# Performance work log

Measured on AMD Instinct MI355X. Metric: run time of the kernel, lower is better.

## Reference

```python
import jax, jax.numpy as jnp
import numpy as np

PATCH = 15  # box-filter kernel size (odd -> SAME padding == padding=PATCH//2, stride 1)


def _box_filter(x, k):
    """All-ones kxk conv2d, stride 1, zero pad k//2. x: (N,1,H,W).
    The ones kernel is separable: ones(k,k) = ones(k,1) @ ones(1,k)."""
    dn = ('NCHW', 'OIHW', 'NCHW')
    kh = jnp.ones((1, 1, k, 1), x.dtype)
    kw = jnp.ones((1, 1, 1, k), x.dtype)
    x = jax.lax.conv_general_dilated(x, kh, (1, 1), 'SAME', dimension_numbers=dn)
    x = jax.lax.conv_general_dilated(x, kw, (1, 1), 'SAME', dimension_numbers=dn)
    return x


def _rgb_to_yuv420(rgb):
    """rgb: (N,3,H,W) -> y:(N,H,W), u,v:(N,H/2,W/2) (2x2 avg-pooled chroma)."""
    r, g, b = rgb[:, 0], rgb[:, 1], rgb[:, 2]
    y = 0.299 * r + 0.587 * g + 0.114 * b
    u = -0.169 * r - 0.331 * g + 0.5 * b + 128.0
    v = 0.5 * r - 0.46 * g - 0.04 * b + 128.0
    n, h, w = u.shape
    u = u.reshape(n, h // 2, 2, w // 2, 2).mean(axis=(2, 4))
    v = v.reshape(n, h // 2, 2, w // 2, 2).mean(axis=(2, 4))
    return y, u, v


def _filtered_channels(img, k):
    y, u, v = _rgb_to_yuv420(img)
    return (_box_filter(y[:, None], k),
            _box_filter(u[:, None], k),
            _box_filter(v[:, None], k))


def setup_inputs() -> dict:
    key = jax.random.key(0)
    k1, k2 = jax.random.split(key)
    input_ = jax.random.uniform(k1, (16, 3, 512, 512), dtype=jnp.float32)
    target = jax.random.uniform(k2, (16, 3, 512, 512), dtype=jnp.float32)
    return {"input": input_, "target": target}


def reference(input, target):
    yi, ui, vi = _filtered_channels(input, PATCH)
    yt, ut, vt = _filtered_channels(target, PATCH)
    mse = lambda a, b: jnp.mean((a - b) ** 2)
    return mse(yi, yt) + mse(ui, ut) + mse(vi, vt)
```

## Files before the change

kernel.cpp:

```cpp
#include <hip/hip_runtime.h>

#define NIMG 16
#define H 512
#define W 512
#define CH 256
#define CW 256
#define HALF 7

__global__ void diff_hbox_kernel(const float* __restrict__ in, const float* __restrict__ tgt,
                                 float* __restrict__ hY, float* __restrict__ hUV) {
    __shared__ float sY0[W + 16], sY1[W + 16], sU[CW + 16], sV[CW + 16];
    const int tid = threadIdx.x;
    const int cy = blockIdx.x & (CH - 1);
    const int n  = blockIdx.x >> 8;

    if (tid < 8) {
        sY0[tid] = 0.f; sY0[W + 8 + tid] = 0.f;
        sY1[tid] = 0.f; sY1[W + 8 + tid] = 0.f;
        sU[tid] = 0.f;  sU[CW + 8 + tid] = 0.f;
        sV[tid] = 0.f;  sV[CW + 8 + tid] = 0.f;
    }

    const size_t plane = (size_t)H * W;
    const float* pi = in  + (size_t)n * 3 * plane;
    const float* pt = tgt + (size_t)n * 3 * plane;

    const int y0 = cy << 1;
    const int x0 = tid << 1;
    const size_t o0 = (size_t)y0 * W + x0;
    const size_t o1 = o0 + W;

    float2 ir0 = *(const float2*)(pi + o0);
    float2 ir1 = *(const float2*)(pi + o1);
    float2 ig0 = *(const float2*)(pi + plane + o0);
    float2 ig1 = *(const float2*)(pi + plane + o1);
    float2 ib0 = *(const float2*)(pi + 2 * plane + o0);
    float2 ib1 = *(const float2*)(pi + 2 * plane + o1);

    float2 tr0 = *(const float2*)(pt + o0);
    float2 tr1 = *(const float2*)(pt + o1);
    float2 tg0 = *(const float2*)(pt + plane + o0);
    float2 tg1 = *(const float2*)(pt + plane + o1);
    float2 tb0 = *(const float2*)(pt + 2 * plane + o0);
    float2 tb1 = *(const float2*)(pt + 2 * plane + o1);

    float dr00 = ir0.x - tr0.x, dr01 = ir0.y - tr0.y;
    float dr10 = ir1.x - tr1.x, dr11 = ir1.y - tr1.y;
    float dg00 = ig0.x - tg0.x, dg01 = ig0.y - tg0.y;
    float dg10 = ig1.x - tg1.x, dg11 = ig1.y - tg1.y;
    float db00 = ib0.x - tb0.x, db01 = ib0.y - tb0.y;
    float db10 = ib1.x - tb1.x, db11 = ib1.y - tb1.y;

    sY0[8 + x0]     = 0.299f * dr00 + 0.587f * dg00 + 0.114f * db00;
    sY0[8 + x0 + 1] = 0.299f * dr01 + 0.587f * dg01 + 0.114f * db01;
    sY1[8 + x0]     = 0.299f * dr10 + 0.587f * dg10 + 0.114f * db10;
    sY1[8 + x0 + 1] = 0.299f * dr11 + 0.587f * dg11 + 0.114f * db11;

    float sr = dr00 + dr01 + dr10 + dr11;
    float sg = dg00 + dg01 + dg10 + dg11;
    float sb = db00 + db01 + db10 + db11;
    sU[8 + tid] = (-0.169f * sr - 0.331f * sg + 0.5f * sb) * 0.25f;
    sV[8 + tid] = ( 0.5f   * sr - 0.46f  * sg - 0.04f * sb) * 0.25f;

    __syncthreads();

    {
        const int row = tid >> 7;
        const int xb  = (tid & 127) << 2;
        const float* srow = row ? sY1 : sY0;
        float s = 0.f;
#pragma unroll
        for (int j = 1; j <= 15; ++j) s += srow[xb + j];
        float4 o;
        o.x = s; s += srow[xb + 16] - srow[xb + 1];
        o.y = s; s += srow[xb + 17] - srow[xb + 2];
        o.z = s; s += srow[xb + 18] - srow[xb + 3];
        o.w = s;
        *(float4*)(hY + ((size_t)n * H + y0 + row) * W + xb) = o;
    }

    {
        const int uv = tid >> 7;
        const int t  = tid & 127;
        const int xb = t << 1;
        const float* srow = uv ? sV : sU;
        float s = 0.f;
#pragma unroll
        for (int j = 1; j <= 15; ++j) s += srow[xb + j];
        float2 o;
        o.x = s; s += srow[xb + 16] - srow[xb + 1];
        o.y = s;
        const size_t p = (size_t)(n * 2 + uv);
        *(float2*)(hUV + (p * CH + cy) * CW + xb) = o;
    }
}

__global__ void vbox_sq_partial_kernel(const float* __restrict__ hY,
                                       const float* __restrict__ hUV,
                                       int gY, float invY, float invC,
                                       float* __restrict__ partials) {
    const int b = blockIdx.x;
    const float* src; int wShift, hMask; float inv; int idx;
    if (b < gY) {
        src = hY; wShift = 9; hMask = H - 1; inv = invY;
        idx = b * 256 + threadIdx.x;
    } else {
        src = hUV; wShift = 8; hMask = CH - 1; inv = invC;
        idx = (b - gY) * 256 + threadIdx.x;
    }
    const int y = (idx >> wShift) & hMask;
    const float* col = src + (idx - (y << wShift));
    float s = 0.f;
#pragma unroll
    for (int t = -HALF; t <= HALF; ++t) {
        int yy = y + t;
        int yc = min(max(yy, 0), hMask);
        float v = col[(size_t)yc << wShift];
        s += (yy == yc) ? v : 0.f;
    }
    float val = s * s;

    for (int o = 32; o > 0; o >>= 1) val += __shfl_down(val, o, 64);
    __shared__ float partial[4];
    const int lane = threadIdx.x & 63, wid = threadIdx.x >> 6;
    if (lane == 0) partial[wid] = val;
    __syncthreads();
    if (threadIdx.x == 0) {
        float t = partial[0] + partial[1] + partial[2] + partial[3];
        partials[b] = t * inv;
    }
}

__global__ void final_reduce_kernel(const float* __restrict__ partials, int n,
                                    float* __restrict__ out) {
    float s = 0.f;
    for (int i = threadIdx.x; i < n; i += 1024) s += partials[i];
    for (int o = 32; o > 0; o >>= 1) s += __shfl_down(s, o, 64);
    __shared__ float partial[16];
    const int lane = threadIdx.x & 63, wid = threadIdx.x >> 6;
    if (lane == 0) partial[wid] = s;
    __syncthreads();
    if (threadIdx.x == 0) {
        float t = 0.f;
#pragma unroll
        for (int i = 0; i < 16; ++i) t += partial[i];
        *out = t;
    }
}

extern "C" void kernel_launch(void* const* d_in, const int* in_sizes, int n_in,
                              void* d_out, int out_size, void* d_ws, size_t ws_size,
                              hipStream_t stream) {
    const float* input  = (const float*)d_in[0];
    const float* target = (const float*)d_in[1];
    float* out = (float*)d_out;

    const size_t yElems = (size_t)NIMG * H * W;
    const size_t cElems = (size_t)NIMG * CH * CW;

    float* ws = (float*)d_ws;
    float* hY       = ws;
    float* hUV      = hY + yElems;
    float* partials = hUV + 2 * cElems;

    const int gY  = (int)(yElems / 256);
    const int gUV = (int)(2 * cElems / 256);
    const int nPart = gY + gUV;

    diff_hbox_kernel<<<NIMG * CH, 256, 0, stream>>>(input, target, hY, hUV);

    vbox_sq_partial_kernel<<<gY + gUV, 256, 0, stream>>>(
        hY, hUV, gY, 1.0f / (float)yElems, 1.0f / (float)cElems, partials);

    final_reduce_kernel<<<1, 1024, 0, stream>>>(partials, nPart, out);
}
```

Measured before the change: 150.0 us.

## Store intermediates as bf16 and fuse vertical box with last-block reduction

The horizontally filtered intermediates are now stored as bf16, which halves the workspace traffic between the two passes. The vertical box pass becomes a running-sum sweep over 128-row chunks per column in only 192 blocks, instead of 15 reads per output element. The separate final reduce kernel is replaced by an atomic counter and last-block reduction, plus a memset of the counter. This trades precision in the intermediates and leaves the vertical pass with low parallelism and a serial dependency down each column.

```diff
diff --git a/kernel.cpp b/kernel.cpp
--- a/kernel.cpp
+++ b/kernel.cpp
@@ -7,8 +7,18 @@
 #define CW 256
 #define HALF 7
 
+static __device__ __forceinline__ unsigned short f2bf(float f) {
+    unsigned u = __float_as_uint(f);
+    u += 0x7FFFu + ((u >> 16) & 1u);
+    return (unsigned short)(u >> 16);
+}
+static __device__ __forceinline__ float bf2f(unsigned short h) {
+    return __uint_as_float(((unsigned)h) << 16);
+}
+
 __global__ void diff_hbox_kernel(const float* __restrict__ in, const float* __restrict__ tgt,
-                                 float* __restrict__ hY, float* __restrict__ hUV) {
+                                 unsigned short* __restrict__ hY,
+                                 unsigned short* __restrict__ hUV) {
     __shared__ float sY0[W + 16], sY1[W + 16], sU[CW + 16], sV[CW + 16];
     const int tid = threadIdx.x;
     const int cy = blockIdx.x & (CH - 1);
@@ -71,12 +81,12 @@
         float s = 0.f;
 #pragma unroll
         for (int j = 1; j <= 15; ++j) s += srow[xb + j];
-        float4 o;
-        o.x = s; s += srow[xb + 16] - srow[xb + 1];
-        o.y = s; s += srow[xb + 17] - srow[xb + 2];
-        o.z = s; s += srow[xb + 18] - srow[xb + 3];
-        o.w = s;
-        *(float4*)(hY + ((size_t)n * H + y0 + row) * W + xb) = o;
+        ushort4 o;
+        o.x = f2bf(s); s += srow[xb + 16] - srow[xb + 1];
+        o.y = f2bf(s); s += srow[xb + 17] - srow[xb + 2];
+        o.z = f2bf(s); s += srow[xb + 18] - srow[xb + 3];
+        o.w = f2bf(s);
+        *(ushort4*)(hY + ((size_t)n * H + y0 + row) * W + xb) = o;
     }
 
     {
@@ -87,64 +97,90 @@
         float s = 0.f;
 #pragma unroll
         for (int j = 1; j <= 15; ++j) s += srow[xb + j];
-        float2 o;
-        o.x = s; s += srow[xb + 16] - srow[xb + 1];
-        o.y = s;
+        ushort2 o;
+        o.x = f2bf(s); s += srow[xb + 16] - srow[xb + 1];
+        o.y = f2bf(s);
         const size_t p = (size_t)(n * 2 + uv);
-        *(float2*)(hUV + (p * CH + cy) * CW + xb) = o;
-    }
-}
-
-__global__ void vbox_sq_partial_kernel(const float* __restrict__ hY,
-                                       const float* __restrict__ hUV,
-                                       int gY, float invY, float invC,
-                                       float* __restrict__ partials) {
+        *(ushort2*)(hUV + (p * CH + cy) * CW + xb) = o;
+    }
+}
+
+#define NBLK 192
+__global__ void vbox_finish_kernel(const unsigned short* __restrict__ hY,
+                                   const unsigned short* __restrict__ hUV,
+                                   float invY, float invC,
+                                   float* __restrict__ partials,
+                                   unsigned* __restrict__ counter,
+                                   float* __restrict__ out) {
     const int b = blockIdx.x;
-    const float* src; int wShift, hMask; float inv; int idx;
-    if (b < gY) {
-        src = hY; wShift = 9; hMask = H - 1; inv = invY;
-        idx = b * 256 + threadIdx.x;
+    float acc = 0.f;
+    if (b < 128) {
+        const int img   = b >> 3;
+        const int strip = (b >> 2) & 1;
+        const int chunk = b & 3;
+        const int x = (strip << 8) + threadIdx.x;
+        const unsigned short* col = hY + ((size_t)img << 18) + x;
+        const int y0 = chunk << 7;
+        float s = 0.f;
+#pragma unroll
+        for (int t = -HALF; t <= HALF; ++t) {
+            int yy = y0 + t;
+            s += ((unsigned)yy < (unsigned)H) ? bf2f(col[yy << 9]) : 0.f;
+        }
+        for (int i = 0; i < 128; ++i) {
+            const int y = y0 + i;
+            acc += s * s;
+            const int ya = y + HALF + 1, yr = y - HALF;
+            float va = ((unsigned)ya < (unsigned)H) ? bf2f(col[ya << 9]) : 0.f;
+            float vr = ((unsigned)yr < (unsigned)H) ? bf2f(col[yr << 9]) : 0.f;
+            s += va - vr;
+        }
+        acc *= invY;
     } else {
-        src = hUV; wShift = 8; hMask = CH - 1; inv = invC;
-        idx = (b - gY) * 256 + threadIdx.x;
-    }
-    const int y = (idx >> wShift) & hMask;
-    const float* col = src + (idx - (y << wShift));
-    float s = 0.f;
-#pragma unroll
-    for (int t = -HALF; t <= HALF; ++t) {
-        int yy = y + t;
-        int yc = min(max(yy, 0), hMask);
-        float v = col[(size_t)yc << wShift];
-        s += (yy == yc) ? v : 0.f;
-    }
-    float val = s * s;
-
-    for (int o = 32; o > 0; o >>= 1) val += __shfl_down(val, o, 64);
-    __shared__ float partial[4];
+        const int bb = b - 128;
+        const int plane = bb >> 1;
+        const int chunk = bb & 1;
+        const int x = threadIdx.x;
+        const unsigned short* col = hUV + ((size_t)plane << 16) + x;
+        const int y0 = chunk << 7;
+        float s = 0.f;
+#pragma unroll
+        for (int t = -HALF; t <= HALF; ++t) {
+            int yy = y0 + t;
+            s += ((unsigned)yy < (unsigned)CH) ? bf2f(col[yy << 8]) : 0.f;
+        }
+        for (int i = 0; i < 128; ++i) {
+            const int y = y0 + i;
+            acc += s * s;
+            const int ya = y + HALF + 1, yr = y - HALF;
+            float va = ((unsigned)ya < (unsigned)CH) ? bf2f(col[ya << 8]) : 0.f;
+            float vr = ((unsigned)yr < (unsigned)CH) ? bf2f(col[yr << 8]) : 0.f;
+            s += va - vr;
+        }
+        acc *= invC;
+    }
+
+    for (int o = 32; o > 0; o >>= 1) acc += __shfl_down(acc, o, 64);
+    __shared__ float part[4];
+    __shared__ bool amLast;
     const int lane = threadIdx.x & 63, wid = threadIdx.x >> 6;
-    if (lane == 0) partial[wid] = val;
+    if (lane == 0) part[wid] = acc;
     __syncthreads();
     if (threadIdx.x == 0) {
-        float t = partial[0] + partial[1] + partial[2] + partial[3];
-        partials[b] = t * inv;
-    }
-}
-
-__global__ void final_reduce_kernel(const float* __restrict__ partials, int n,
-                                    float* __restrict__ out) {
-    float s = 0.f;
-    for (int i = threadIdx.x; i < n; i += 1024) s += partials[i];
-    for (int o = 32; o > 0; o >>= 1) s += __shfl_down(s, o, 64);
-    __shared__ float partial[16];
-    const int lane = threadIdx.x & 63, wid = threadIdx.x >> 6;
-    if (lane == 0) partial[wid] = s;
+        partials[b] = part[0] + part[1] + part[2] + part[3];
+        __threadfence();
+        unsigned prev = atomicAdd(counter, 1u);
+        amLast = (prev == NBLK - 1);
+    }
     __syncthreads();
-    if (threadIdx.x == 0) {
-        float t = 0.f;
-#pragma unroll
-        for (int i = 0; i < 16; ++i) t += partial[i];
-        *out = t;
+    if (amLast) {
+        __threadfence();
+        float s = (threadIdx.x < NBLK) ? partials[threadIdx.x] : 0.f;
+        for (int o = 32; o > 0; o >>= 1) s += __shfl_down(s, o, 64);
+        __syncthreads();
+        if (lane == 0) part[wid] = s;
+        __syncthreads();
+        if (threadIdx.x == 0) *out = part[0] + part[1] + part[2] + part[3];
     }
 }
 
@@ -158,19 +194,16 @@
     const size_t yElems = (size_t)NIMG * H * W;
     const size_t cElems = (size_t)NIMG * CH * CW;
 
-    float* ws = (float*)d_ws;
-    float* hY       = ws;
-    float* hUV      = hY + yElems;
-    float* partials = hUV + 2 * cElems;
-
-    const int gY  = (int)(yElems / 256);
-    const int gUV = (int)(2 * cElems / 256);
-    const int nPart = gY + gUV;
+    unsigned short* hY  = (unsigned short*)d_ws;
+    unsigned short* hUV = hY + yElems;
+    float* partials = (float*)(hUV + 2 * cElems);
+    unsigned* counter = (unsigned*)(partials + NBLK);
+
+    hipMemsetAsync(counter, 0, sizeof(unsigned), stream);
 
     diff_hbox_kernel<<<NIMG * CH, 256, 0, stream>>>(input, target, hY, hUV);
 
-    vbox_sq_partial_kernel<<<gY + gUV, 256, 0, stream>>>(
-        hY, hUV, gY, 1.0f / (float)yElems, 1.0f / (float)cElems, partials);
-
-    final_reduce_kernel<<<1, 1024, 0, stream>>>(partials, nPart, out);
-}
+    vbox_finish_kernel<<<NBLK, 256, 0, stream>>>(
+        hY, hUV, 1.0f / (float)yElems, 1.0f / (float)cElems,
+        partials, counter, out);
+}
```

Result: slower. 171.7 us (+14.4%).
